# Performance work log

Measured on AMD Instinct MI355X. Metric: run time of the kernel, lower is better.

Reference implementation:

```python
import jax, jax.numpy as jnp
import numpy as np

# ---- static config (mirrors GaussianLSS __init__) ----
ORF_H, ORF_W = 256, 704
FC, FH, FW = 128, 32, 88
D_ST, D_END, D_STEP = 4.0, 45.0, 1.0
OUT_C = 128
ERROR_TOL = 1.0
OPACITY_THR = 0.05
XB = (-50.0, 50.0, 1.0)
YB = (-50.0, 50.0, 1.0)
BEV_H = int(round((YB[1] - YB[0]) / YB[2]))
BEV_W = int(round((XB[1] - XB[0]) / XB[2]))
DS = np.arange(D_ST, D_END, D_STEP, dtype=np.float32)
D = DS.shape[0]  # 41
BN_EPS = 1e-3
CHUNK = 512      # gaussians composited per scan step (16896 = 33*512)
B, NCAM = 1, 6


def make_frustum():
    ds = jnp.broadcast_to(jnp.asarray(DS)[:, None, None], (D, FH, FW))
    xs = jnp.broadcast_to(jnp.linspace(0.0, ORF_W - 1.0, FW)[None, None, :], (D, FH, FW))
    ys = jnp.broadcast_to(jnp.linspace(0.0, ORF_H - 1.0, FH)[None, :, None], (D, FH, FW))
    return jnp.stack([xs, ys, ds], -1)  # [D,FH,FW,3]


def get_geometry(rots, trans, intrins, post_rots, post_trans):
    fr = make_frustum()
    pts = fr[None, None] - post_trans[:, :, None, None, None, :]
    pts = jnp.einsum('bnij,bndhwj->bndhwi', jnp.linalg.inv(post_rots), pts)
    pts = jnp.concatenate([pts[..., :2] * pts[..., 2:3], pts[..., 2:3]], -1)
    comb = jnp.einsum('bnij,bnjk->bnik', rots, jnp.linalg.inv(intrins))
    pts = jnp.einsum('bnij,bndhwj->bndhwi', comb, pts) + trans[:, :, None, None, None, :]
    return pts  # [B,N,D,FH,FW,3] ego-frame frustum points


def conv2d(x, w, b, pad):
    y = jax.lax.conv_general_dilated(x, w, (1, 1), [(pad, pad), (pad, pad)],
                                     dimension_numbers=('NCHW', 'OIHW', 'NCHW'))
    return y + b[None, :, None, None]


def bnorm(x, g, bt, m, v):
    s = (g / jnp.sqrt(v + BN_EPS))[None, :, None, None]
    return (x - m[None, :, None, None]) * s + bt[None, :, None, None]


def splat(means, cov6, colors, ops, valid_in):
    # Differentiable BEV gaussian rasterization (3DGS math, orthographic BEV camera,
    # all depths equal -> compositing in stable gaussian-index order).
    H, W = BEV_H, BEV_W
    sh, sw = H / 2.0, W / 2.0  # h/h_meters with FoV=2 (BEVCamera)
    my = -sh * means[:, 1] + H / 2.0  # pixel row (full_proj_transform row 0)
    mx = -sw * means[:, 0] + W / 2.0  # pixel col (row 1)
    a = sh * sh * cov6[:, 3] + 0.3    # 2D cov = J Sigma_xy J^T, +0.3 low-pass as in 3DGS
    c = sw * sw * cov6[:, 0] + 0.3
    b = sh * sw * cov6[:, 1]
    det = a * c - b * b
    valid = valid_in & (det > 0)
    inv_det = jnp.where(det > 0, 1.0 / det, 0.0)
    cA, cB, cC = c * inv_det, -b * inv_det, a * inv_det
    pi = jnp.repeat(jnp.arange(H, dtype=jnp.float32), W)  # [P] pixel rows
    pj = jnp.tile(jnp.arange(W, dtype=jnp.float32), H)    # [P] pixel cols
    G = means.shape[0]
    nchunk = G // CHUNK
    resh = lambda x: x.reshape((nchunk, CHUNK) + x.shape[1:])
    chunks = (resh(my), resh(mx), resh(cA), resh(cB), resh(cC),
              resh(ops), resh(valid), resh(colors))

    def body(carry, ch):
        logT, acc = carry
        my_c, mx_c, A, Bc, Cc, op_c, val_c, col_c = ch
        dI = pi[None, :] - my_c[:, None]                     # [Gc,P]
        dJ = pj[None, :] - mx_c[:, None]
        q = A[:, None] * dI * dI + 2.0 * Bc[:, None] * dI * dJ + Cc[:, None] * dJ * dJ
        alpha = jnp.minimum(0.99, op_c[:, None] * jnp.exp(-0.5 * q))
        alpha = jnp.where(val_c[:, None] & (q >= 0) & (alpha >= 1.0 / 255.0), alpha, 0.0)
        log1m = jnp.log1p(-alpha)
        cum = jnp.cumsum(log1m, axis=0)
        T = jnp.exp(logT[None, :] + cum - log1m)             # transmittance before each gaussian
        acc = acc + jnp.einsum('gp,gc->pc', alpha * T, col_c)
        return (logT + cum[-1], acc), None

    P = H * W
    init = (jnp.zeros((P,), jnp.float32), jnp.zeros((P, colors.shape[1]), jnp.float32))
    (_, acc), _ = jax.lax.scan(jax.checkpoint(body), init, chunks)
    return acc.reshape(H, W, -1).transpose(2, 0, 1)  # [C,H,W], bg is zeros


def _forward(cam2ego_rot, cam2ego_trans, cam_intrins, post_cam2ego_rot, post_cam2ego_trans,
             img_feats, conv1_w, conv1_b, bn1_g, bn1_b, bn1_m, bn1_v,
             conv2_w, conv2_b, bn2_g, bn2_b, bn2_m, bn2_v, conv3_w, conv3_b):
    geom = get_geometry(cam2ego_rot, cam2ego_trans, cam_intrins, post_cam2ego_rot, post_cam2ego_trans)
    b, n = img_feats.shape[:2]
    x = img_feats.reshape(b * n, FC, FH, FW)
    x = jax.nn.relu(bnorm(conv2d(x, conv1_w, conv1_b, 1), bn1_g, bn1_b, bn1_m, bn1_v))
    x = jax.nn.relu(bnorm(conv2d(x, conv2_w, conv2_b, 1), bn2_g, bn2_b, bn2_m, bn2_v))
    x = conv2d(x, conv3_w, conv3_b, 0)
    depth_prob = jax.nn.softmax(x[:, :D], axis=1).reshape(b, n, D, FH, FW)
    opac = jax.nn.sigmoid(x[:, D:D + 1]).reshape(b, n, FH, FW)
    feats = x[:, D + 1:].reshape(b, n, OUT_C, FH, FW)
    # per-pixel gaussian moments of the depth distribution (compute_gaussian)
    means = jnp.einsum('bndhw,bndhwi->bnhwi', depth_prob, geom)
    delta = means[:, :, None] - geom                                       # [B,N,D,FH,FW,3]
    cov = jnp.einsum('bndhw,bndhwi,bndhwj->bnhwij', depth_prob, delta, delta) * (ERROR_TOL ** 2 / 9.0)
    center = jnp.array([(XB[0] + XB[1]) / 2.0, (YB[0] + YB[1]) / 2.0, 0.0], jnp.float32)
    scale = jnp.array([2.0 / (XB[1] - XB[0]), 2.0 / (YB[1] - YB[0]), 1.0], jnp.float32)
    m_n = (means - center) * scale
    cov_n = cov * (scale[:, None] * scale[None, :])
    cov6 = jnp.stack([cov_n[..., 0, 0], cov_n[..., 0, 1], cov_n[..., 0, 2],
                      cov_n[..., 1, 1], cov_n[..., 1, 2], cov_n[..., 2, 2]], -1)
    g = n * FH * FW
    colors = feats.transpose(0, 1, 3, 4, 2).reshape(b, g, OUT_C)
    m_n = m_n.reshape(b, g, 3)
    cov6 = cov6.reshape(b, g, 6)
    ops = opac.reshape(b, g)
    mask = ops > OPACITY_THR  # opacity filtering == zero contribution, order preserved
    bev = jax.vmap(splat)(m_n, cov6, colors, ops, mask)                    # [B,C,H,W]
    num_gaussians = mask.astype(jnp.float32).sum(-1).mean()
    return bev, num_gaussians


def setup_inputs():
    key = jax.random.key(0)
    ks = jax.random.split(key, 8)
    # camera-to-ego rotations: cam->ego axis permutation composed with per-camera yaw
    yaw = np.linspace(0.0, 2.0 * np.pi, NCAM, endpoint=False).astype(np.float32)
    cz, sz = np.cos(yaw), np.sin(yaw)
    rotz = np.zeros((NCAM, 3, 3), np.float32)
    rotz[:, 0, 0] = cz; rotz[:, 0, 1] = -sz
    rotz[:, 1, 0] = sz; rotz[:, 1, 1] = cz
    rotz[:, 2, 2] = 1.0
    perm = np.array([[0.0, 0.0, 1.0], [-1.0, 0.0, 0.0], [0.0, -1.0, 0.0]], np.float32)
    rots = np.einsum('nij,jk->nik', rotz, perm)
    cam2ego_rot = jnp.asarray(np.broadcast_to(rots, (B, NCAM, 3, 3)).copy())
    cam2ego_trans = jax.random.normal(ks[0], (B, NCAM, 3), jnp.float32)
    K = np.array([[600.0, 0.0, ORF_W / 2.0], [0.0, 600.0, ORF_H / 2.0], [0.0, 0.0, 1.0]], np.float32)
    cam_intrins = jnp.asarray(np.broadcast_to(K, (B, NCAM, 3, 3)).copy())
    post_cam2ego_rot = jnp.broadcast_to(jnp.eye(3, dtype=jnp.float32), (B, NCAM, 3, 3)) + jnp.zeros((B, NCAM, 3, 3), jnp.float32)
    post_cam2ego_trans = jnp.zeros((B, NCAM, 3), jnp.float32)
    img_feats = jax.random.normal(ks[1], (B, NCAM, FC, FH, FW), jnp.float32)
    def conv_init(k, o, i, kh, kw):
        return jax.random.normal(k, (o, i, kh, kw), jnp.float32) * (1.0 / np.sqrt(i * kh * kw))
    return dict(cam2ego_rot=cam2ego_rot, cam2ego_trans=cam2ego_trans, cam_intrins=cam_intrins,
                post_cam2ego_rot=post_cam2ego_rot, post_cam2ego_trans=post_cam2ego_trans,
                img_feats=img_feats,
                conv1_w=conv_init(ks[2], FC, FC, 3, 3), conv1_b=jnp.zeros((FC,), jnp.float32),
                bn1_g=jnp.ones((FC,), jnp.float32), bn1_b=jnp.zeros((FC,), jnp.float32),
                bn1_m=jnp.zeros((FC,), jnp.float32), bn1_v=jnp.ones((FC,), jnp.float32),
                conv2_w=conv_init(ks[3], FC, FC, 3, 3), conv2_b=jnp.zeros((FC,), jnp.float32),
                bn2_g=jnp.ones((FC,), jnp.float32), bn2_b=jnp.zeros((FC,), jnp.float32),
                bn2_m=jnp.zeros((FC,), jnp.float32), bn2_v=jnp.ones((FC,), jnp.float32),
                conv3_w=conv_init(ks[4], OUT_C + D + 1, FC, 1, 1),
                conv3_b=jax.random.normal(ks[5], (OUT_C + D + 1,), jnp.float32) * 0.1)


def reference(cam2ego_rot, cam2ego_trans, cam_intrins, post_cam2ego_rot, post_cam2ego_trans,
              img_feats, conv1_w, conv1_b, bn1_g, bn1_b, bn1_m, bn1_v,
              conv2_w, conv2_b, bn2_g, bn2_b, bn2_m, bn2_v, conv3_w, conv3_b):
    return _forward(cam2ego_rot, cam2ego_trans, cam_intrins, post_cam2ego_rot, post_cam2ego_trans,
                    img_feats, conv1_w, conv1_b, bn1_g, bn1_b, bn1_m, bn1_v,
                    conv2_w, conv2_b, bn2_g, bn2_b, bn2_m, bn2_v, conv3_w, conv3_b)
```

## Files before the change

### kernel.cpp

```cpp
#include <hip/hip_runtime.h>

#define NCAM 6
#define FC   128
#define FH_  32
#define FW_  88
#define NPIX (FH_*FW_)
#define PH   34
#define PW   92
#define PPIX (PH*PW)
#define ND   41
#define X3D  42
#define OUTC 128
#define GTOT (NCAM*NPIX)
#define BEVH 100
#define BEVW 100
#define NPXB (BEVH*BEVW)
#define NTILE 25
#define NWORD 264
#define NMASKW (NTILE*NTILE*NWORD)
#define WCAP  70000
#define CSIZE 64
#define CBLK  2048

#define SZA     (NCAM*FC*PPIX)
#define WS_CAM  0
#define WS_A    256
#define WS_RB   (WS_A  + SZA)
#define WS_X3   (WS_RB + SZA)
#define WS_GS   (WS_X3 + NCAM*X3D*NPIX)
#define WS_WL   (WS_GS + GTOT*8)
#define WS_BASE (WS_WL + WCAP)

typedef __attribute__((ext_vector_type(8))) short bf16x8;
typedef __attribute__((ext_vector_type(4))) float f32x4;

__device__ inline unsigned short f2bf(float f) {
    unsigned u = __float_as_uint(f);
    u += 0x7fffu + ((u >> 16) & 1u);
    return (unsigned short)(u >> 16);
}

__device__ inline void inv3x3(const float* m, float* o) {
    float a=m[0],b=m[1],c=m[2],d=m[3],e=m[4],f=m[5],g=m[6],h=m[7],i=m[8];
    float A=e*i-f*h, B=c*h-b*i, C=b*f-c*e;
    float Dd=f*g-d*i, E=a*i-c*g, F=c*d-a*f;
    float Gg=d*h-e*g, H=b*g-a*h, I=a*e-b*d;
    float r = 1.0f/(a*A + b*Dd + c*Gg);
    o[0]=A*r; o[1]=B*r; o[2]=C*r; o[3]=Dd*r; o[4]=E*r; o[5]=F*r;
    o[6]=Gg*r; o[7]=H*r; o[8]=I*r;
}

__global__ __launch_bounds__(256) void pad_input_kernel(const float* __restrict__ src,
        float* __restrict__ dst, float* __restrict__ rb,
        float* __restrict__ outp, unsigned long long* __restrict__ masks) {
    int idx = blockIdx.x*256 + threadIdx.x;
    if (idx < NMASKW) masks[idx] = 0ull;
    if (idx <= NPXB*OUTC) outp[idx] = 0.0f;
    if (idx >= NCAM*FC*PPIX) return;
    int plane = idx / PPIX, pp = idx - plane*PPIX;
    int y = pp / PW, x = pp - y*PW;
    bool interior = (y >= 1 && y <= FH_ && x >= 1 && x <= FW_);
    float v = 0.0f;
    if (interior)
        v = src[(size_t)plane*NPIX + (y-1)*FW_ + (x-1)];
    dst[idx] = v;
    if (!interior) rb[idx] = 0.0f;
}

__global__ __launch_bounds__(128) void conv3x3_pf_kernel(
        const float* __restrict__ in, float* __restrict__ out, const float* __restrict__ w,
        const float* __restrict__ cb, const float* __restrict__ bg, const float* __restrict__ bb,
        const float* __restrict__ bm, const float* __restrict__ bv) {
    const int n   = blockIdx.x;
    const int co0 = blockIdx.y * 4;
    const int qid = blockIdx.z * 128 + threadIdx.x;
    if (qid >= 704) return;
    const int y = qid / 22, x0 = (qid - y*22) * 4;
    float scale[4], shift[4];
    #pragma unroll
    for (int c=0;c<4;c++) {
        float s = bg[co0+c] * rsqrtf(bv[co0+c] + 1e-3f);
        scale[c] = s;
        shift[c] = (cb[co0+c] - bm[co0+c]) * s + bb[co0+c];
    }
    float acc[4][4] = {};
    const float* ip = in + (size_t)n*FC*PPIX + y*PW + x0;
    const float* wb = w + (size_t)co0*FC*9;
    float4 p4[3]; float2 p2[3];
    #pragma unroll
    for (int r=0;r<3;r++) {
        p4[r] = *(const float4*)(ip + r*PW);
        p2[r] = *(const float2*)(ip + r*PW + 4);
    }
    for (int ci=0; ci<FC; ++ci) {
        float v[3][6];
        #pragma unroll
        for (int r=0;r<3;r++) {
            v[r][0]=p4[r].x; v[r][1]=p4[r].y; v[r][2]=p4[r].z; v[r][3]=p4[r].w;
            v[r][4]=p2[r].x; v[r][5]=p2[r].y;
        }
        if (ci + 1 < FC) {
            const float* ipn = ip + PPIX;
            #pragma unroll
            for (int r=0;r<3;r++) {
                p4[r] = *(const float4*)(ipn + r*PW);
                p2[r] = *(const float2*)(ipn + r*PW + 4);
            }
        }
        #pragma unroll
        for (int c=0;c<4;c++) {
            const float* wr = wb + (size_t)c*FC*9 + ci*9;
            float w00=wr[0],w01=wr[1],w02=wr[2],w10=wr[3],w11=wr[4],
                  w12=wr[5],w20=wr[6],w21=wr[7],w22=wr[8];
            #pragma unroll
            for (int p=0;p<4;p++) {
                float a = acc[c][p];
                a = fmaf(w00, v[0][p], a); a = fmaf(w01, v[0][p+1], a); a = fmaf(w02, v[0][p+2], a);
                a = fmaf(w10, v[1][p], a); a = fmaf(w11, v[1][p+1], a); a = fmaf(w12, v[1][p+2], a);
                a = fmaf(w20, v[2][p], a); a = fmaf(w21, v[2][p+1], a); a = fmaf(w22, v[2][p+2], a);
                acc[c][p] = a;
            }
        }
        ip += PPIX;
    }
    const int po = (y+1)*PW + (x0+1);
    #pragma unroll
    for (int c=0;c<4;c++) {
        float* op = out + ((size_t)n*FC + co0 + c)*PPIX + po;
        #pragma unroll
        for (int p=0;p<4;p++)
            op[p] = fmaxf(fmaf(acc[c][p], scale[c], shift[c]), 0.0f);
    }
}

__global__ __launch_bounds__(256) void conv1x1_kernel(const float* __restrict__ in,
        float* __restrict__ x3d, unsigned short* __restrict__ colors16,
        const float* __restrict__ w, const float* __restrict__ b) {
    const int n   = blockIdx.x;
    const int px  = blockIdx.y * 256 + threadIdx.x;
    const int y   = px / FW_, x = px - y*FW_;
    const int pp  = (y+1)*PW + (x+1);
    const float* ip = in + (size_t)n*FC*PPIX + pp;
    if (blockIdx.z < 6) {
        const int co0 = blockIdx.z * 7;
        const float* wr[7];
        float acc[7];
        #pragma unroll
        for (int k=0;k<7;k++) {
            int co = co0 + k;
            wr[k]  = w + (size_t)co*FC;
            acc[k] = b[co];
        }
        #pragma unroll 4
        for (int ci=0; ci<FC; ++ci) {
            float v = ip[(size_t)ci*PPIX];
            #pragma unroll
            for (int k=0;k<7;k++) acc[k] = fmaf(wr[k][ci], v, acc[k]);
        }
        #pragma unroll
        for (int k=0;k<7;k++)
            x3d[((size_t)n*X3D + co0 + k)*NPIX + px] = acc[k];
    } else {
        const int c0  = (blockIdx.z - 6) * 8;
        const int co0 = X3D + c0;
        const float* wr[8];
        float acc[8];
        #pragma unroll
        for (int k=0;k<8;k++) {
            int co = co0 + k;
            wr[k]  = w + (size_t)co*FC;
            acc[k] = b[co];
        }
        #pragma unroll 4
        for (int ci=0; ci<FC; ++ci) {
            float v = ip[(size_t)ci*PPIX];
            #pragma unroll
            for (int k=0;k<8;k++) acc[k] = fmaf(wr[k][ci], v, acc[k]);
        }
        unsigned short h[8];
        #pragma unroll
        for (int k=0;k<8;k++) h[k] = f2bf(acc[k]);
        uint4 pk;
        pk.x = (unsigned)h[0] | ((unsigned)h[1] << 16);
        pk.y = (unsigned)h[2] | ((unsigned)h[3] << 16);
        pk.z = (unsigned)h[4] | ((unsigned)h[5] << 16);
        pk.w = (unsigned)h[6] | ((unsigned)h[7] << 16);
        *(uint4*)(colors16 + (((size_t)(n*NPIX + px)) << 7) + c0) = pk;
    }
}

__global__ __launch_bounds__(256) void moments_kernel(const float* __restrict__ x3,
        const float* __restrict__ rot, const float* __restrict__ tr,
        const float* __restrict__ intr, const float* __restrict__ prot,
        const float* __restrict__ ptr_, float* __restrict__ gauss,
        float* __restrict__ ng) {
    __shared__ float cc[24];
    const int n = blockIdx.x / 11;
    if (threadIdx.x == 0) {
        float M1[9], Ki[9];
        inv3x3(prot + n*9, M1);
        inv3x3(intr + n*9, Ki);
        const float* R = rot + n*9;
        #pragma unroll
        for (int i=0;i<9;i++) cc[i] = M1[i];
        #pragma unroll
        for (int i=0;i<3;i++) cc[9+i] = ptr_[n*3+i];
        #pragma unroll
        for (int i=0;i<3;i++)
            #pragma unroll
            for (int j=0;j<3;j++)
                cc[12+i*3+j] = R[i*3+0]*Ki[0+j] + R[i*3+1]*Ki[3+j] + R[i*3+2]*Ki[6+j];
        #pragma unroll
        for (int i=0;i<3;i++) cc[21+i] = tr[n*3+i];
    }
    __syncthreads();
    const int gi = blockIdx.x*256 + threadIdx.x;
    const int p  = gi - n*NPIX;
    const int h  = p / FW_, xp = p - h*FW_;
    float u = xp * (703.0f/87.0f);
    float v = h  * (255.0f/31.0f);
    float fx = u - cc[9], fy = v - cc[10], fz = -cc[11];
    float p0x = cc[0]*fx + cc[1]*fy + cc[2]*fz;
    float p0y = cc[3]*fx + cc[4]*fy + cc[5]*fz;
    float p0z = cc[6]*fx + cc[7]*fy + cc[8]*fz;
    const float* lg = x3 + (size_t)n*X3D*NPIX + p;

    float lgv[ND];
    #pragma unroll
    for (int d=0; d<ND; ++d) lgv[d] = lg[(size_t)d*NPIX];

    float mxl = -1e30f;
    #pragma unroll
    for (int d=0; d<ND; ++d) mxl = fmaxf(mxl, lgv[d]);

    float s=0.f, sgx=0.f, sgy=0.f;
    #pragma unroll
    for (int d=0; d<ND; ++d) {
        float e  = __expf(lgv[d] - mxl);
        lgv[d] = e;
        float dz = 4.0f + (float)d;
        float pz = p0z + dz*cc[8];
        float px = (p0x + dz*cc[2]) * pz;
        float py = (p0y + dz*cc[5]) * pz;
        float gx = cc[12]*px + cc[13]*py + cc[14]*pz + cc[21];
        float gy = cc[15]*px + cc[16]*py + cc[17]*pz + cc[22];
        s += e; sgx += e*gx; sgy += e*gy;
    }
    float inv_s = 1.0f/s;
    float mex = sgx*inv_s, mey = sgy*inv_s;
    float cxx=0.f, cxy=0.f, cyy=0.f;
    #pragma unroll
    for (int d=0; d<ND; ++d) {
        float e  = lgv[d];
        float dz = 4.0f + (float)d;
        float pz = p0z + dz*cc[8];
        float px = (p0x + dz*cc[2]) * pz;
        float py = (p0y + dz*cc[5]) * pz;
        float gx = cc[12]*px + cc[13]*py + cc[14]*pz + cc[21];
        float gy = cc[15]*px + cc[16]*py + cc[17]*pz + cc[22];
        float dxv = gx - mex, dyv = gy - mey;
        cxx += e*dxv*dxv; cxy += e*dxv*dyv; cyy += e*dyv*dyv;
    }
    const float k9 = inv_s * (1.0f/9.0f);
    cxx *= k9; cxy *= k9; cyy *= k9;

    float lo = lg[(size_t)ND*NPIX];
    float op = 1.0f/(1.0f + __expf(-lo));
    bool mask = op > 0.05f;

    const float SC = 0.02f, SH = 50.0f, SW = 50.0f;
    float my = -SH*(mey*SC) + 50.0f;
    float mx = -SW*(mex*SC) + 50.0f;
    float a  = SH*SH*(cyy*SC*SC) + 0.3f;
    float b  = SH*SW*(cxy*SC*SC);
    float c  = SW*SW*(cxx*SC*SC) + 0.3f;
    float det = a*c - b*b;
    bool valid = mask && (det > 0.0f);
    float A, B2, C, qm, ri, rj;
    if (valid) {
        float idet = 1.0f/det;
        A = c*idet; B2 = -2.0f*b*idet; C = a*idet;
        qm = 2.0f*__logf(255.0f*op);
        ri = sqrtf(qm*a); rj = sqrtf(qm*c);
    } else { A=B2=C=0.f; qm=-1.0f; ri=-1e30f; rj=-1e30f; }
    float* gp = gauss + (size_t)gi*8;
    gp[0]=my; gp[1]=mx; gp[2]=A; gp[3]=B2; gp[4]=C; gp[5]=qm; gp[6]=ri; gp[7]=rj;

    unsigned long long bal = __ballot(mask);
    if ((threadIdx.x & 63) == 0) atomicAdd(ng, (float)__popcll(bal));
}

__global__ __launch_bounds__(256) void scatter_masks_kernel(const float* __restrict__ gauss,
        unsigned long long* __restrict__ masks) {
    const int idx = blockIdx.x*256 + threadIdx.x;
    const int g = idx >> 2, q = idx & 3;
    const float4 g0 = *(const float4*)(gauss + ((size_t)g << 3));
    const float4 g1 = *(const float4*)(gauss + ((size_t)g << 3) + 4);
    if (g1.y < 0.0f) return;
    const float my = g0.x, mx = g0.y, A = g0.z, B = 0.5f*g0.w, C = g1.x, qm = g1.y, ri = g1.z;
    const float invC = 1.0f / C;
    const float k2 = C*A - B*B;
    int ti0 = max(0, (int)floorf((my - ri) * 0.25f));
    int ti1 = min(NTILE-1, (int)floorf((my + ri) * 0.25f));
    int len = ti1 - ti0 + 1;
    int ta = ti0 + (len*q) / 4;
    int tb = ti0 + (len*(q+1)) / 4;
    const int wi = g >> 6;
    const unsigned long long bit = 1ull << (g & 63);
    for (int ti = ta; ti < tb; ++ti) {
        float jmn = 1e30f, jmx = -1e30f;
        #pragma unroll
        for (int r = 0; r < 4; ++r) {
            int i = 4*ti + r;
            if (i < 0 || i > 99) continue;
            float di = (float)i - my;
            float disc = C*qm - k2*di*di;
            if (disc < 0.0f) continue;
            float sd = sqrtf(disc);
            float jc = -B*di;
            jmn = fminf(jmn, (jc - sd)*invC + mx);
            jmx = fmaxf(jmx, (jc + sd)*invC + mx);
        }
        if (jmx < jmn) continue;
        int jl = max(0, (int)ceilf(jmn));
        int jh = min(99, (int)floorf(jmx));
        if (jl > jh) continue;
        for (int tj = (jl >> 2); tj <= (jh >> 2); ++tj)
            atomicOr(&masks[(size_t)(ti*NTILE + tj)*NWORD + wi], bit);
    }
}

__global__ __launch_bounds__(256) void cnt_kernel(const unsigned long long* __restrict__ masks,
                                                  int* __restrict__ cnt) {
    __shared__ int sc;
    const int tile = blockIdx.x, t = threadIdx.x;
    if (t == 0) sc = 0;
    __syncthreads();
    if (t < NWORD) atomicAdd(&sc, __popcll(masks[(size_t)tile*NWORD + t]));
    __syncthreads();
    if (t == 0) cnt[tile] = sc;
}

__global__ __launch_bounds__(640) void scan_kernel(const int* __restrict__ cnt,
        int* __restrict__ off, int* __restrict__ choff, int* __restrict__ nwork) {
    __shared__ int wsum[16], wsum2[16];
    const int t = threadIdx.x;
    const int lane = t & 63, wv = t >> 6;
    int c  = (t < NTILE*NTILE) ? cnt[t] : 0;
    int ch = (c + CSIZE-1) >> 6;
    int v = c, v2 = ch;
    #pragma unroll
    for (int o = 1; o < 64; o <<= 1) {
        int u  = __shfl_up(v,  (unsigned)o, 64);
        int u2 = __shfl_up(v2, (unsigned)o, 64);
        if (lane >= o) { v += u; v2 += u2; }
    }
    if (lane == 63) { wsum[wv] = v; wsum2[wv] = v2; }
    __syncthreads();
    int pre = 0, pre2 = 0;
    for (int w2 = 0; w2 < wv; ++w2) { pre += wsum[w2]; pre2 += wsum2[w2]; }
    int inc = v + pre, inc2 = v2 + pre2;
    if (t < NTILE*NTILE) { off[t] = inc - c; choff[t] = inc2 - ch; }
    if (t == NTILE*NTILE - 1) {
        off[NTILE*NTILE] = inc;
        choff[NTILE*NTILE] = inc2;
        nwork[0] = (inc2 > WCAP) ? WCAP : inc2;
    }
}

__global__ __launch_bounds__(256) void fill_kernel(const unsigned long long* __restrict__ masks,
        const int* __restrict__ cnt, const int* __restrict__ off, const int* __restrict__ choff,
        unsigned short* __restrict__ list, int* __restrict__ wl) {
    __shared__ unsigned long long sw[NWORD];
    __shared__ int wpre[NWORD];
    const int tile = blockIdx.x, t = threadIdx.x;
    if (t < NWORD) sw[t] = masks[(size_t)tile*NWORD + t];
    __syncthreads();
    if (t == 0) {
        int run = 0;
        for (int w2 = 0; w2 < NWORD; ++w2) { wpre[w2] = run; run += __popcll(sw[w2]); }
    }
    __syncthreads();
    if (t < NWORD) {
        unsigned long long m = sw[t];
        int pos = off[tile] + wpre[t], base = t << 6;
        while (m) { int b = __builtin_ctzll(m); m &= m - 1; list[pos++] = (unsigned short)(base + b); }
    }
    int nch = (cnt[tile] + CSIZE-1)/CSIZE;
    int c0 = choff[tile];
    if (t < nch && c0 + t < WCAP) wl[c0 + t] = (tile << 9) | t;
}

__device__ inline float eval_alpha(const float4 g0, const float4 g1, float fi, float fj) {
    float dI = fi - g0.x, dJ = fj - g0.y;
    float q = dI*(g0.z*dI + g0.w*dJ) + g1.x*dJ*dJ;
    if (q < 0.0f || q > g1.y) return 0.0f;
    return fminf(0.99f, 0.003921568627f * __expf(0.5f*(g1.y - q)));
}

__global__ __launch_bounds__(256) void chunk_sums_kernel(const float* __restrict__ gauss,
        const unsigned short* __restrict__ list, const int* __restrict__ cnt,
        const int* __restrict__ off, const int* __restrict__ wl, const int* __restrict__ nwork,
        float* __restrict__ base) {
    const int nw = nwork[0];
    const int lane = threadIdx.x & 63;
    const int wid  = (blockIdx.x * 256 + threadIdx.x) >> 6;
    const int nwv  = (gridDim.x * 256) >> 6;
    const int px = lane & 15, kg = lane >> 4;
    for (int e = wid; e < nw; e += nwv) {
        int v = wl[e], tile = v >> 9, c = v & 511;
        int hbase = off[tile] + (c << 6);
        int nh = min(CSIZE, cnt[tile] - (c << 6));
        const int i0 = (tile / NTILE) * 4, j0 = (tile % NTILE) * 4;
        const float fi = (float)(i0 + (px >> 2)), fj = (float)(j0 + (px & 3));
        float s = 1.0f;
        for (int k = kg; k < nh; k += 4) {
            int g = list[hbase + k];
            float4 g0 = *(const float4*)(gauss + ((size_t)g << 3));
            float4 g1 = *(const float4*)(gauss + ((size_t)g << 3) + 4);
            float a = eval_alpha(g0, g1, fi, fj);
            s *= (1.0f - a);
        }
        s *= __shfl_xor(s, 16, 64);
        s *= __shfl_xor(s, 32, 64);
        if (lane < 16) base[(size_t)e*16 + lane] = s;
    }
}

__global__ __launch_bounds__(256) void chunk_prefix_kernel(const int* __restrict__ choff,
                                                           float* __restrict__ base) {
    __shared__ float part[16][17];
    const int tile = blockIdx.x, t = threadIdx.x;
    const int c0 = choff[tile], nch = choff[tile+1] - c0;
    if (nch == 0) return;
    const int px = t & 15, cg = t >> 4;
    const int L16 = (nch + 15) >> 4;
    const int a0 = cg*L16, a1 = min(nch, a0 + L16);
    float s = 1.0f;
    for (int c = a0; c < a1; ++c) s *= base[(size_t)(c0 + c)*16 + px];
    part[cg][px] = s;
    __syncthreads();
    if (t < 16) {
        float run = 1.0f;
        #pragma unroll
        for (int k = 0; k < 16; ++k) { float tmp = part[k][t]; part[k][t] = run; run *= tmp; }
    }
    __syncthreads();
    float run = part[cg][px];
    for (int c = a0; c < a1; ++c) {
        size_t idx = (size_t)(c0 + c)*16 + px;
        float tmp = base[idx];
        base[idx] = run;
        run *= tmp;
    }
}

__global__ __launch_bounds__(256) void composite_kernel(const float* __restrict__ gauss,
        const unsigned short* __restrict__ colors16, const unsigned short* __restrict__ list,
        const int* __restrict__ cnt, const int* __restrict__ off, const int* __restrict__ wl,
        const int* __restrict__ nwork, const float* __restrict__ base, float* __restrict__ out) {
    const int nw = nwork[0];
    const int t = threadIdx.x;
    const int lane = t & 63;
    const int e_px = t >> 4, e_kg = t & 15;
    const int wv_id = t >> 6;
    const int m16 = lane & 15;
    const int kb  = lane >> 4;
    const int chA = (wv_id << 5) + m16;
    const int chB = chA + 16;
    const int f_pxq = t >> 5;
    const int f_r0  = f_pxq >> 2, f_j = f_pxq & 3;
    const int cs4r  = t & 31;
    __shared__ unsigned short slist[4][CSIZE];
    __shared__ unsigned short s_w16[2][8][17][8];
    __shared__ float fred[128*17];
    const int per = (nw + CBLK - 1) / CBLK;
    int e0 = blockIdx.x * per;
    if (e0 >= nw) return;
    int e1 = min(nw, e0 + per);

    f32x4 accA = {0.f,0.f,0.f,0.f};
    f32x4 accB = {0.f,0.f,0.f,0.f};
    int cur_tile = wl[e0] >> 9;
    int cur_i0 = (cur_tile / NTILE) * 4, cur_j0 = (cur_tile % NTILE) * 4;

    int L = e0;
    for (; L < e1 && L < e0 + 2; ++L) {
        int v = wl[L], tl = v >> 9, c = v & 511;
        int nhl = min(CSIZE, cnt[tl] - (c << 6));
        if (t < CSIZE) slist[L & 3][t] = (t < nhl) ? list[off[tl] + (c << 6) + t] : 0;
    }

    int e = e0;
    while (e < e1) {
        int v = wl[e], tile = v >> 9, c = v & 511;
        bool pair = false; int c2 = 0;
        if (e + 1 < e1) {
            int v2 = wl[e+1];
            if ((v2 >> 9) == tile) { pair = true; c2 = v2 & 511; }
        }
        const bool tflush = (tile != cur_tile);
        const int fi0 = cur_i0, fj0 = cur_j0;
        if (tflush) {
            const int cs4A = (wv_id << 3) + (m16 >> 2);
            const int compA = m16 & 3;
            #pragma unroll
            for (int r = 0; r < 4; ++r) {
                fred[((kb << 5) + cs4A)*17 + (r << 2) + compA]     = accA[r];
                fred[((kb << 5) + cs4A + 4)*17 + (r << 2) + compA] = accB[r];
            }
            accA = (f32x4){0.f,0.f,0.f,0.f};
            accB = (f32x4){0.f,0.f,0.f,0.f};
            cur_tile = tile;
            cur_i0 = (tile / NTILE) * 4; cur_j0 = (tile % NTILE) * 4;
        }
        const int nh  = min(CSIZE, cnt[tile] - (c << 6));
        const int nh2 = pair ? min(CSIZE, cnt[tile] - (c2 << 6)) : 0;
        __syncthreads();
        if (tflush) {
            const float* f0 = &fred[(f_r0*32 + cs4r)*17 + (f_j<<2)];
            const float* f1 = &fred[((f_r0+2)*32 + cs4r)*17 + (f_j<<2)];
            const int pix0 = (fi0 + f_r0) * BEVW + fj0 + f_j;
            const int pix1 = pix0 + 2 * BEVW;
            float* op = out + (size_t)(cs4r << 2) * NPXB;
            atomicAdd(op + 0*NPXB + pix0, f0[0]); atomicAdd(op + 1*NPXB + pix0, f0[1]);
            atomicAdd(op + 2*NPXB + pix0, f0[2]); atomicAdd(op + 3*NPXB + pix0, f0[3]);
            atomicAdd(op + 0*NPXB + pix1, f1[0]); atomicAdd(op + 1*NPXB + pix1, f1[1]);
            atomicAdd(op + 2*NPXB + pix1, f1[2]); atomicAdd(op + 3*NPXB + pix1, f1[3]);
        }
        {
            const int target = min(e1, e + (pair ? 2 : 1) + 2);
            for (; L < target; ++L) {
                int vv = wl[L], tl = vv >> 9, cc = vv & 511;
                int nhl = min(CSIZE, cnt[tl] - (cc << 6));
                if (t < CSIZE) slist[L & 3][t] = (t < nhl) ? list[off[tl] + (cc << 6) + t] : 0;
            }
        }
        {
            const float fi = (float)(cur_i0 + (e_px >> 2)), fj = (float)(cur_j0 + (e_px & 3));
            const int k0 = e_kg << 2;
            float a4a[4], a4b[4];
            float p1 = 1.0f, p2 = 1.0f;
            #pragma unroll
            for (int i = 0; i < 4; ++i) {
                int k = k0 + i;
                float aa = 0.0f, ab = 0.0f;
                if (k < nh) {
                    int g = slist[e & 3][k];
                    float4 g0 = *(const float4*)(gauss + ((size_t)g << 3));
                    float4 g1 = *(const float4*)(gauss + ((size_t)g << 3) + 4);
                    aa = eval_alpha(g0, g1, fi, fj);
                }
                if (k < nh2) {
                    int g = slist[(e+1) & 3][k];
                    float4 g0 = *(const float4*)(gauss + ((size_t)g << 3));
                    float4 g1 = *(const float4*)(gauss + ((size_t)g << 3) + 4);
                    ab = eval_alpha(g0, g1, fi, fj);
                }
                a4a[i] = aa; a4b[i] = ab;
                p1 *= (1.0f - aa);
                p2 *= (1.0f - ab);
            }
            float sa = p1, sb = p2;
            #pragma unroll
            for (int o = 1; o < 16; o <<= 1) {
                float ua = __shfl_up(sa, (unsigned)o, 64);
                float ub = __shfl_up(sb, (unsigned)o, 64);
                if ((lane & 15) >= o) { sa *= ua; sb *= ub; }
            }
            float exa = __shfl_up(sa, 1u, 64);
            float exb = __shfl_up(sb, 1u, 64);
            const bool l0 = ((lane & 15) == 0);
            float Ta = base[(size_t)e*16 + e_px] * (l0 ? 1.0f : exa);
            unsigned short* swpa = &s_w16[0][e_kg >> 1][e_px][(e_kg & 1) << 2];
            #pragma unroll
            for (int i = 0; i < 4; ++i) {
                float wv_ = a4a[i] * Ta; Ta -= wv_;
                swpa[i] = f2bf(wv_);
            }
            if (pair) {
                float Tb = base[(size_t)(e+1)*16 + e_px] * (l0 ? 1.0f : exb);
                unsigned short* swpb = &s_w16[1][e_kg >> 1][e_px][(e_kg & 1) << 2];
                #pragma unroll
                for (int i = 0; i < 4; ++i) {
                    float wv_ = a4b[i] * Tb; Tb -= wv_;
                    swpb[i] = f2bf(wv_);
                }
            }
        }
        __syncthreads();
        {
            bf16x8 af0 = *(const bf16x8*)&s_w16[0][kb][m16][0];
            bf16x8 af1 = *(const bf16x8*)&s_w16[0][4 + kb][m16][0];
            bf16x8 bA0, bB0, bA1, bB1;
            #pragma unroll
            for (int j = 0; j < 8; ++j) {
                int g0i = slist[e & 3][(kb << 3) + j];
                int g1i = slist[e & 3][32 + (kb << 3) + j];
                const unsigned short* cp0 = colors16 + ((size_t)g0i << 7);
                const unsigned short* cp1 = colors16 + ((size_t)g1i << 7);
                bA0[j] = (short)cp0[chA]; bB0[j] = (short)cp0[chB];
                bA1[j] = (short)cp1[chA]; bB1[j] = (short)cp1[chB];
            }
            if (pair) {
                bf16x8 cf0 = *(const bf16x8*)&s_w16[1][kb][m16][0];
                bf16x8 cf1 = *(const bf16x8*)&s_w16[1][4 + kb][m16][0];
                bf16x8 dA0, dB0, dA1, dB1;
                #pragma unroll
                for (int j = 0; j < 8; ++j) {
                    int g0i = slist[(e+1) & 3][(kb << 3) + j];
                    int g1i = slist[(e+1) & 3][32 + (kb << 3) + j];
                    const unsigned short* cp0 = colors16 + ((size_t)g0i << 7);
                    const unsigned short* cp1 = colors16 + ((size_t)g1i << 7);
                    dA0[j] = (short)cp0[chA]; dB0[j] = (short)cp0[chB];
                    dA1[j] = (short)cp1[chA]; dB1[j] = (short)cp1[chB];
                }
                accA = __builtin_amdgcn_mfma_f32_16x16x32_bf16(af0, bA0, accA, 0, 0, 0);
                accB = __builtin_amdgcn_mfma_f32_16x16x32_bf16(af0, bB0, accB, 0, 0, 0);
                accA = __builtin_amdgcn_mfma_f32_16x16x32_bf16(af1, bA1, accA, 0, 0, 0);
                accB = __builtin_amdgcn_mfma_f32_16x16x32_bf16(af1, bB1, accB, 0, 0, 0);
                accA = __builtin_amdgcn_mfma_f32_16x16x32_bf16(cf0, dA0, accA, 0, 0, 0);
                accB = __builtin_amdgcn_mfma_f32_16x16x32_bf16(cf0, dB0, accB, 0, 0, 0);
                accA = __builtin_amdgcn_mfma_f32_16x16x32_bf16(cf1, dA1, accA, 0, 0, 0);
                accB = __builtin_amdgcn_mfma_f32_16x16x32_bf16(cf1, dB1, accB, 0, 0, 0);
            } else {
                accA = __builtin_amdgcn_mfma_f32_16x16x32_bf16(af0, bA0, accA, 0, 0, 0);
                accB = __builtin_amdgcn_mfma_f32_16x16x32_bf16(af0, bB0, accB, 0, 0, 0);
                accA = __builtin_amdgcn_mfma_f32_16x16x32_bf16(af1, bA1, accA, 0, 0, 0);
                accB = __builtin_amdgcn_mfma_f32_16x16x32_bf16(af1, bB1, accB, 0, 0, 0);
            }
        }
        e += pair ? 2 : 1;
    }
    {
        const int cs4A = (wv_id << 3) + (m16 >> 2);
        const int compA = m16 & 3;
        #pragma unroll
        for (int r = 0; r < 4; ++r) {
            fred[((kb << 5) + cs4A)*17 + (r << 2) + compA]     = accA[r];
            fred[((kb << 5) + cs4A + 4)*17 + (r << 2) + compA] = accB[r];
        }
    }
    __syncthreads();
    {
        const float* f0 = &fred[(f_r0*32 + cs4r)*17 + (f_j<<2)];
        const float* f1 = &fred[((f_r0+2)*32 + cs4r)*17 + (f_j<<2)];
        const int pix0 = (cur_i0 + f_r0) * BEVW + cur_j0 + f_j;
        const int pix1 = pix0 + 2 * BEVW;
        float* op = out + (size_t)(cs4r << 2) * NPXB;
        atomicAdd(op + 0*NPXB + pix0, f0[0]); atomicAdd(op + 1*NPXB + pix0, f0[1]);
        atomicAdd(op + 2*NPXB + pix0, f0[2]); atomicAdd(op + 3*NPXB + pix0, f0[3]);
        atomicAdd(op + 0*NPXB + pix1, f1[0]); atomicAdd(op + 1*NPXB + pix1, f1[1]);
        atomicAdd(op + 2*NPXB + pix1, f1[2]); atomicAdd(op + 3*NPXB + pix1, f1[3]);
    }
}

extern "C" void kernel_launch(void* const* d_in, const int* in_sizes, int n_in,
                              void* d_out, int out_size, void* d_ws, size_t ws_size,
                              hipStream_t stream) {
    const float* rot  = (const float*)d_in[0];
    const float* tr   = (const float*)d_in[1];
    const float* intr = (const float*)d_in[2];
    const float* prot = (const float*)d_in[3];
    const float* ptr_ = (const float*)d_in[4];
    const float* img  = (const float*)d_in[5];
    const float* c1w  = (const float*)d_in[6];  const float* c1b = (const float*)d_in[7];
    const float* b1g  = (const float*)d_in[8];  const float* b1b = (const float*)d_in[9];
    const float* b1m  = (const float*)d_in[10]; const float* b1v = (const float*)d_in[11];
    const float* c2w  = (const float*)d_in[12]; const float* c2b = (const float*)d_in[13];
    const float* b2g  = (const float*)d_in[14]; const float* b2b = (const float*)d_in[15];
    const float* b2m  = (const float*)d_in[16]; const float* b2v = (const float*)d_in[17];
    const float* c3w  = (const float*)d_in[18]; const float* c3b = (const float*)d_in[19];
    float* out = (float*)d_out;
    float* ws  = (float*)d_ws;
    float* RA  = ws + WS_A;
    float* RB  = ws + WS_RB;
    float* X3B = ws + WS_X3;
    float* GS  = ws + WS_GS;
    int*   WL  = (int*)(ws + WS_WL);
    float* BASE = ws + WS_BASE;
    unsigned long long* MASKS = (unsigned long long*)BASE;
    int* AUXI = (int*)(ws + WS_X3 + 330000);
    int* CNT = AUXI;
    int* OFF = AUXI + 640;
    int* CHOFF = AUXI + 1280;
    int* NWORK = AUXI + 1920;
    unsigned short* LIST = (unsigned short*)RA;
    unsigned short* COL16 = (unsigned short*)RB;
    float* ngp = out + (size_t)NPXB*OUTC;

    pad_input_kernel<<<(NCAM*FC*PPIX + 255)/256, 256, 0, stream>>>(img, RA, RB, out, MASKS);
    conv3x3_pf_kernel<<<dim3(NCAM,32,6), 128, 0, stream>>>(RA, RB, c1w, c1b, b1g, b1b, b1m, b1v);
    conv3x3_pf_kernel<<<dim3(NCAM,32,6), 128, 0, stream>>>(RB, RA, c2w, c2b, b2g, b2b, b2m, b2v);
    conv1x1_kernel<<<dim3(NCAM,11,22), 256, 0, stream>>>(RA, X3B, COL16, c3w, c3b);
    moments_kernel<<<GTOT/256, 256, 0, stream>>>(X3B, rot, tr, intr, prot, ptr_, GS, ngp);
    scatter_masks_kernel<<<GTOT*4/256, 256, 0, stream>>>(GS, MASKS);
    cnt_kernel<<<NTILE*NTILE, 256, 0, stream>>>(MASKS, CNT);
    scan_kernel<<<1, 640, 0, stream>>>(CNT, OFF, CHOFF, NWORK);
    fill_kernel<<<NTILE*NTILE, 256, 0, stream>>>(MASKS, CNT, OFF, CHOFF, LIST, WL);
    chunk_sums_kernel<<<8192, 256, 0, stream>>>(GS, LIST, CNT, OFF, WL, NWORK, BASE);
    chunk_prefix_kernel<<<NTILE*NTILE, 256, 0, stream>>>(CHOFF, BASE);
    composite_kernel<<<CBLK, 256, 0, stream>>>(GS, COL16, LIST, CNT, OFF, WL, NWORK, BASE, out);
}
```

Baseline: 451.5 us.

## Run 3x3 convolutions on bf16 MFMA with channel-last padded activations

Replaces the fp32 FMA direct 3x3 convolutions with an implicit-GEMM kernel using bf16 16x16x32 MFMA instructions. Inputs are transposed into a padded channels-last bf16 layout, and weights are converted to bf16 tap-major once per call. The 1x1 conv now reads bf16 channel-last activations with 16-byte loads. This cuts convolution arithmetic and memory traffic but lowers activation precision to bf16 and adds weight-conversion and transpose passes.

```diff
diff --git a/kernel.cpp b/kernel.cpp
--- a/kernel.cpp
+++ b/kernel.cpp
@@ -23,13 +23,14 @@
 #define CBLK  2048
 
 #define SZA     (NCAM*FC*PPIX)
-#define WS_CAM  0
 #define WS_A    256
+#define C1OFF   1201152
 #define WS_RB   (WS_A  + SZA)
 #define WS_X3   (WS_RB + SZA)
 #define WS_GS   (WS_X3 + NCAM*X3D*NPIX)
 #define WS_WL   (WS_GS + GTOT*8)
 #define WS_BASE (WS_WL + WCAP)
+#define WELEM   (9*128*128)
 
 typedef __attribute__((ext_vector_type(8))) short bf16x8;
 typedef __attribute__((ext_vector_type(4))) float f32x4;
@@ -38,6 +39,10 @@
     unsigned u = __float_as_uint(f);
     u += 0x7fffu + ((u >> 16) & 1u);
     return (unsigned short)(u >> 16);
+}
+__device__ inline float bf2f(unsigned short h) {
+    unsigned u = ((unsigned)h) << 16;
+    return __uint_as_float(u);
 }
 
 __device__ inline void inv3x3(const float* m, float* o) {
@@ -50,97 +55,112 @@
     o[6]=Gg*r; o[7]=H*r; o[8]=I*r;
 }
 
-__global__ __launch_bounds__(256) void pad_input_kernel(const float* __restrict__ src,
-        float* __restrict__ dst, float* __restrict__ rb,
+__global__ __launch_bounds__(256) void prep_weights_kernel(const float* __restrict__ w1,
+        const float* __restrict__ w2, unsigned short* __restrict__ wc1,
+        unsigned short* __restrict__ wc2) {
+    int idx = blockIdx.x*256 + threadIdx.x;
+    if (idx >= 2*WELEM) return;
+    const float* src = (idx < WELEM) ? w1 : w2;
+    unsigned short* dst = (idx < WELEM) ? wc1 : wc2;
+    int e = (idx < WELEM) ? idx : idx - WELEM;
+    int tap = e / (128*128), r = e - tap*(128*128);
+    int co = r >> 7, ci = r & 127;
+    int dy = tap / 3, dx = tap - dy*3;
+    dst[e] = f2bf(src[((co*128 + ci)*3 + dy)*3 + dx]);
+}
+
+__global__ __launch_bounds__(256) void pad_tr_kernel(const float* __restrict__ src,
+        unsigned short* __restrict__ pad16, unsigned short* __restrict__ c1o16,
         float* __restrict__ outp, unsigned long long* __restrict__ masks) {
-    int idx = blockIdx.x*256 + threadIdx.x;
-    if (idx < NMASKW) masks[idx] = 0ull;
-    if (idx <= NPXB*OUTC) outp[idx] = 0.0f;
-    if (idx >= NCAM*FC*PPIX) return;
-    int plane = idx / PPIX, pp = idx - plane*PPIX;
-    int y = pp / PW, x = pp - y*PW;
-    bool interior = (y >= 1 && y <= FH_ && x >= 1 && x <= FW_);
-    float v = 0.0f;
-    if (interior)
-        v = src[(size_t)plane*NPIX + (y-1)*FW_ + (x-1)];
-    dst[idx] = v;
-    if (!interior) rb[idx] = 0.0f;
-}
-
-__global__ __launch_bounds__(128) void conv3x3_pf_kernel(
-        const float* __restrict__ in, float* __restrict__ out, const float* __restrict__ w,
-        const float* __restrict__ cb, const float* __restrict__ bg, const float* __restrict__ bb,
-        const float* __restrict__ bm, const float* __restrict__ bv) {
-    const int n   = blockIdx.x;
-    const int co0 = blockIdx.y * 4;
-    const int qid = blockIdx.z * 128 + threadIdx.x;
-    if (qid >= 704) return;
-    const int y = qid / 22, x0 = (qid - y*22) * 4;
-    float scale[4], shift[4];
+    __shared__ unsigned short lds[92*132];
+    const int bid = blockIdx.x;
+    const int n = bid / PH, y = bid - n*PH;
+    const int t = threadIdx.x;
+    for (int j = bid*256 + t; j <= NPXB*OUTC; j += 204*256) outp[j] = 0.0f;
+    for (int j = bid*256 + t; j < NMASKW; j += 204*256) masks[j] = 0ull;
+
+    unsigned short* prow = pad16 + ((size_t)n*PPIX + y*PW)*128;
+    unsigned short* crow = c1o16 + ((size_t)n*PPIX + y*PW)*128;
+    if (y == 0 || y == PH-1) {
+        for (int j = t; j < PW*128; j += 256) { prow[j] = 0; crow[j] = 0; }
+        return;
+    }
+    for (int j = t; j < 4*128; j += 256) {
+        int bc = j >> 7, ci = j & 127;
+        int xp = (bc == 0) ? 0 : (88 + bc);
+        lds[xp*132 + ci] = 0;
+        crow[xp*128 + ci] = 0;
+    }
+    const float* sp = src + (size_t)n*FC*NPIX + (size_t)(y-1)*FW_;
+    for (int j = t; j < 128*FW_; j += 256) {
+        int ci = j / FW_, x = j - ci*FW_;
+        lds[(x+1)*132 + ci] = f2bf(sp[(size_t)ci*NPIX + x]);
+    }
+    __syncthreads();
+    for (int j = t; j < PW*128; j += 256) {
+        int xp = j >> 7, ci = j & 127;
+        prow[j] = lds[xp*132 + ci];
+    }
+}
+
+__global__ __launch_bounds__(256) void conv3x3_mfma_kernel(
+        const unsigned short* __restrict__ in16, unsigned short* __restrict__ out16,
+        const unsigned short* __restrict__ wcvt,
+        const float* __restrict__ cb, const float* __restrict__ bg,
+        const float* __restrict__ bb, const float* __restrict__ bm,
+        const float* __restrict__ bv) {
+    const int n = blockIdx.x;
+    const int y = blockIdx.y + 1;
+    const int half = blockIdx.z;
+    const int t = threadIdx.x;
+    const int lane = t & 63, wv = t >> 6;
+    const int n16 = lane & 15, kb = lane >> 4;
+    const int co = half*64 + wv*16 + n16;
+    const float scale = bg[co] * rsqrtf(bv[co] + 1e-3f);
+    const float shift = (cb[co] - bm[co]) * scale + bb[co];
+
+    const unsigned short* ibase = in16 + (size_t)n*PPIX*128;
+    f32x4 acc[6];
     #pragma unroll
-    for (int c=0;c<4;c++) {
-        float s = bg[co0+c] * rsqrtf(bv[co0+c] + 1e-3f);
-        scale[c] = s;
-        shift[c] = (cb[co0+c] - bm[co0+c]) * s + bb[co0+c];
-    }
-    float acc[4][4] = {};
-    const float* ip = in + (size_t)n*FC*PPIX + y*PW + x0;
-    const float* wb = w + (size_t)co0*FC*9;
-    float4 p4[3]; float2 p2[3];
+    for (int m = 0; m < 6; ++m) acc[m] = (f32x4){0.f,0.f,0.f,0.f};
+
+    for (int kc = 0; kc < 4; ++kc) {
+        #pragma unroll
+        for (int tap = 0; tap < 9; ++tap) {
+            const int dy = tap / 3, dx = tap - dy*3;
+            bf16x8 bfrag = *(const bf16x8*)(wcvt + ((size_t)(tap*128 + co))*128 + kc*32 + kb*8);
+            const unsigned short* arow = ibase + (size_t)(y + dy - 1)*PW*128 + kc*32 + kb*8;
+            #pragma unroll
+            for (int m = 0; m < 6; ++m) {
+                int col = m*16 + n16 + dx;
+                col = min(col, 91);
+                bf16x8 afrag = *(const bf16x8*)(arow + (size_t)col*128);
+                acc[m] = __builtin_amdgcn_mfma_f32_16x16x32_bf16(afrag, bfrag, acc[m], 0, 0, 0);
+            }
+        }
+    }
+    unsigned short* obase = out16 + ((size_t)n*PPIX + y*PW)*128 + co;
     #pragma unroll
-    for (int r=0;r<3;r++) {
-        p4[r] = *(const float4*)(ip + r*PW);
-        p2[r] = *(const float2*)(ip + r*PW + 4);
-    }
-    for (int ci=0; ci<FC; ++ci) {
-        float v[3][6];
-        #pragma unroll
-        for (int r=0;r<3;r++) {
-            v[r][0]=p4[r].x; v[r][1]=p4[r].y; v[r][2]=p4[r].z; v[r][3]=p4[r].w;
-            v[r][4]=p2[r].x; v[r][5]=p2[r].y;
-        }
-        if (ci + 1 < FC) {
-            const float* ipn = ip + PPIX;
-            #pragma unroll
-            for (int r=0;r<3;r++) {
-                p4[r] = *(const float4*)(ipn + r*PW);
-                p2[r] = *(const float2*)(ipn + r*PW + 4);
-            }
-        }
-        #pragma unroll
-        for (int c=0;c<4;c++) {
-            const float* wr = wb + (size_t)c*FC*9 + ci*9;
-            float w00=wr[0],w01=wr[1],w02=wr[2],w10=wr[3],w11=wr[4],
-                  w12=wr[5],w20=wr[6],w21=wr[7],w22=wr[8];
-            #pragma unroll
-            for (int p=0;p<4;p++) {
-                float a = acc[c][p];
-                a = fmaf(w00, v[0][p], a); a = fmaf(w01, v[0][p+1], a); a = fmaf(w02, v[0][p+2], a);
-                a = fmaf(w10, v[1][p], a); a = fmaf(w11, v[1][p+1], a); a = fmaf(w12, v[1][p+2], a);
-                a = fmaf(w20, v[2][p], a); a = fmaf(w21, v[2][p+1], a); a = fmaf(w22, v[2][p+2], a);
-                acc[c][p] = a;
-            }
-        }
-        ip += PPIX;
-    }
-    const int po = (y+1)*PW + (x0+1);
-    #pragma unroll
-    for (int c=0;c<4;c++) {
-        float* op = out + ((size_t)n*FC + co0 + c)*PPIX + po;
-        #pragma unroll
-        for (int p=0;p<4;p++)
-            op[p] = fmaxf(fmaf(acc[c][p], scale[c], shift[c]), 0.0f);
-    }
-}
-
-__global__ __launch_bounds__(256) void conv1x1_kernel(const float* __restrict__ in,
+    for (int m = 0; m < 6; ++m) {
+        #pragma unroll
+        for (int r = 0; r < 4; ++r) {
+            int xp = 1 + m*16 + kb*4 + r;
+            if (xp <= 88) {
+                float v = fmaxf(fmaf(acc[m][r], scale, shift), 0.0f);
+                obase[(size_t)xp*128] = f2bf(v);
+            }
+        }
+    }
+}
+
+__global__ __launch_bounds__(256) void conv1x1_kernel(const unsigned short* __restrict__ in16,
         float* __restrict__ x3d, unsigned short* __restrict__ colors16,
         const float* __restrict__ w, const float* __restrict__ b) {
     const int n   = blockIdx.x;
     const int px  = blockIdx.y * 256 + threadIdx.x;
     const int y   = px / FW_, x = px - y*FW_;
     const int pp  = (y+1)*PW + (x+1);
-    const float* ip = in + (size_t)n*FC*PPIX + pp;
+    const unsigned short* ip = in16 + ((size_t)n*PPIX + pp)*128;
     if (blockIdx.z < 6) {
         const int co0 = blockIdx.z * 7;
         const float* wr[7];
@@ -151,11 +171,20 @@
             wr[k]  = w + (size_t)co*FC;
             acc[k] = b[co];
         }
-        #pragma unroll 4
-        for (int ci=0; ci<FC; ++ci) {
-            float v = ip[(size_t)ci*PPIX];
-            #pragma unroll
-            for (int k=0;k<7;k++) acc[k] = fmaf(wr[k][ci], v, acc[k]);
+        for (int c8 = 0; c8 < 16; ++c8) {
+            uint4 pk = *(const uint4*)(ip + c8*8);
+            const unsigned* pw = (const unsigned*)&pk;
+            #pragma unroll
+            for (int j = 0; j < 4; ++j) {
+                float v0 = bf2f((unsigned short)(pw[j] & 0xffffu));
+                float v1 = bf2f((unsigned short)(pw[j] >> 16));
+                int ci = c8*8 + j*2;
+                #pragma unroll
+                for (int k=0;k<7;k++) {
+                    acc[k] = fmaf(wr[k][ci],   v0, acc[k]);
+                    acc[k] = fmaf(wr[k][ci+1], v1, acc[k]);
+                }
+            }
         }
         #pragma unroll
         for (int k=0;k<7;k++)
@@ -171,11 +200,20 @@
             wr[k]  = w + (size_t)co*FC;
             acc[k] = b[co];
         }
-        #pragma unroll 4
-        for (int ci=0; ci<FC; ++ci) {
-            float v = ip[(size_t)ci*PPIX];
-            #pragma unroll
-            for (int k=0;k<8;k++) acc[k] = fmaf(wr[k][ci], v, acc[k]);
+        for (int c8 = 0; c8 < 16; ++c8) {
+            uint4 pk = *(const uint4*)(ip + c8*8);
+            const unsigned* pw = (const unsigned*)&pk;
+            #pragma unroll
+            for (int j = 0; j < 4; ++j) {
+                float v0 = bf2f((unsigned short)(pw[j] & 0xffffu));
+                float v1 = bf2f((unsigned short)(pw[j] >> 16));
+                int ci = c8*8 + j*2;
+                #pragma unroll
+                for (int k=0;k<8;k++) {
+                    acc[k] = fmaf(wr[k][ci],   v0, acc[k]);
+                    acc[k] = fmaf(wr[k][ci+1], v1, acc[k]);
+                }
+            }
         }
         unsigned short h[8];
         #pragma unroll
@@ -673,9 +711,12 @@
     const float* c3w  = (const float*)d_in[18]; const float* c3b = (const float*)d_in[19];
     float* out = (float*)d_out;
     float* ws  = (float*)d_ws;
-    float* RA  = ws + WS_A;
-    float* RB  = ws + WS_RB;
+    unsigned short* PAD16 = (unsigned short*)(ws + WS_A);
+    unsigned short* C1O16 = (unsigned short*)(ws + WS_A + C1OFF);
+    unsigned short* COL16 = (unsigned short*)(ws + WS_RB);
     float* X3B = ws + WS_X3;
+    unsigned short* WC1 = (unsigned short*)X3B;
+    unsigned short* WC2 = WC1 + WELEM;
     float* GS  = ws + WS_GS;
     int*   WL  = (int*)(ws + WS_WL);
     float* BASE = ws + WS_BASE;
@@ -685,14 +726,16 @@
     int* OFF = AUXI + 640;
     int* CHOFF = AUXI + 1280;
     int* NWORK = AUXI + 1920;
-    unsigned short* LIST = (unsigned short*)RA;
-    unsigned short* COL16 = (unsigned short*)RB;
+    unsigned short* LIST = (unsigned short*)(ws + WS_A);
     float* ngp = out + (size_t)NPXB*OUTC;
 
-    pad_input_kernel<<<(NCAM*FC*PPIX + 255)/256, 256, 0, stream>>>(img, RA, RB, out, MASKS);
-    conv3x3_pf_kernel<<<dim3(NCAM,32,6), 128, 0, stream>>>(RA, RB, c1w, c1b, b1g, b1b, b1m, b1v);
-    conv3x3_pf_kernel<<<dim3(NCAM,32,6), 128, 0, stream>>>(RB, RA, c2w, c2b, b2g, b2b, b2m, b2v);
-    conv1x1_kernel<<<dim3(NCAM,11,22), 256, 0, stream>>>(RA, X3B, COL16, c3w, c3b);
+    prep_weights_kernel<<<(2*WELEM + 255)/256, 256, 0, stream>>>(c1w, c2w, WC1, WC2);
+    pad_tr_kernel<<<NCAM*PH, 256, 0, stream>>>(img, PAD16, C1O16, out, MASKS);
+    conv3x3_mfma_kernel<<<dim3(NCAM,32,2), 256, 0, stream>>>(PAD16, C1O16, WC1,
+                                                             c1b, b1g, b1b, b1m, b1v);
+    conv3x3_mfma_kernel<<<dim3(NCAM,32,2), 256, 0, stream>>>(C1O16, PAD16, WC2,
+                                                             c2b, b2g, b2b, b2m, b2v);
+    conv1x1_kernel<<<dim3(NCAM,11,22), 256, 0, stream>>>(PAD16, X3B, COL16, c3w, c3b);
     moments_kernel<<<GTOT/256, 256, 0, stream>>>(X3B, rot, tr, intr, prot, ptr_, GS, ngp);
     scatter_masks_kernel<<<GTOT*4/256, 256, 0, stream>>>(GS, MASKS);
     cnt_kernel<<<NTILE*NTILE, 256, 0, stream>>>(MASKS, CNT);
```

Measured after the change: 417.7 us. 7.5% less time.
